# Optimization experiments

Hardware: AMD Instinct MI355X
Metric: run time of the kernel (lower is better)

The kernel has to match this reference:

```python
import jax, jax.numpy as jnp
import numpy as np

GH, GW = 7, 7            # hierarchical grid size
LN_EPS = 1e-5            # torch nn.LayerNorm default eps
NEG = -1e9


def _adaptive_avg_pool2d(x, oh, ow):
    # Replicates torch F.adaptive_avg_pool2d bin boundaries:
    # start=floor(i*H/out), end=ceil((i+1)*H/out). x: (..., H, W)
    H, W = x.shape[-2], x.shape[-1]
    def b(i, n, o):
        return int(np.floor(i * n / o)), int(np.ceil((i + 1) * n / o))
    rows = jnp.stack([x[..., b(i, H, oh)[0]:b(i, H, oh)[1], :].mean(axis=-2)
                      for i in range(oh)], axis=-2)
    out = jnp.stack([rows[..., b(j, W, ow)[0]:b(j, W, ow)[1]].mean(axis=-1)
                     for j in range(ow)], axis=-1)
    return out


def _layernorm(y, gamma, beta):
    mu = y.mean(axis=-1, keepdims=True)
    var = jnp.mean(jnp.square(y - mu), axis=-1, keepdims=True)
    return (y - mu) * jax.lax.rsqrt(var + LN_EPS) * gamma + beta


def setup_inputs() -> dict:
    key = jax.random.key(0)
    ks = jax.random.split(key, 16)
    B, C, H, W = 8, 512, 32, 32
    heads = 8
    s = 0.02
    f32 = jnp.float32
    return {
        "x":    jax.random.normal(ks[0], (B, C, H, W), f32),
        "Wq":   jax.random.normal(ks[1], (C, C), f32) * s,
        "bq":   jnp.zeros((C,), f32),
        "Wk":   jax.random.normal(ks[2], (C, C), f32) * s,
        "bk":   jnp.zeros((C,), f32),
        "Wv":   jax.random.normal(ks[3], (C, C), f32) * s,
        "bv":   jnp.zeros((C,), f32),
        "Wo":   jax.random.normal(ks[4], (C, C), f32) * s,
        "bo":   jnp.zeros((C,), f32),
        "Wsp":  jax.random.normal(ks[5], (heads, C), f32) * s,   # 1x1 conv C->heads
        "bsp":  jnp.zeros((heads,), f32),
        "Wse1": jax.random.normal(ks[6], (C // 16, C), f32) * s, # SE squeeze
        "bse1": jnp.zeros((C // 16,), f32),
        "Wse2": jax.random.normal(ks[7], (C, C // 16), f32) * s, # SE excite
        "bse2": jnp.zeros((C,), f32),
        "gamma": jnp.ones((C,), f32),
        "beta":  jnp.zeros((C,), f32),
    }


def reference(x, Wq, bq, Wk, bk, Wv, bv, Wo, bo, Wsp, bsp,
              Wse1, bse1, Wse2, bse2, gamma, beta):
    B, C, H, W = x.shape
    heads = Wsp.shape[0]
    d = C // heads
    N = H * W

    # --- hierarchical grid mask ---
    sp = jnp.einsum('bchw,nc->bnhw', x, Wsp) + bsp[None, :, None, None]
    m = jax.nn.sigmoid(sp)                               # (B, heads, H, W)
    mg = _adaptive_avg_pool2d(m, GH, GW)
    mg = (mg > 0.5).astype(x.dtype)                      # binarize
    ih = np.floor(np.arange(H) * GH / H).astype(np.int32)  # torch 'nearest'
    iw = np.floor(np.arange(W) * GW / W).astype(np.int32)
    mask = mg[..., ih[:, None], iw[None, :]]             # (B, heads, H, W)

    # --- SE channel gating ---
    pooled = x.mean(axis=(2, 3))                         # (B, C)
    h1 = jax.nn.relu(pooled @ Wse1.T + bse1)
    cw = jax.nn.sigmoid(h1 @ Wse2.T + bse2)              # (B, C)
    xf = (x * cw[:, :, None, None]).reshape(B, C, N).transpose(0, 2, 1)  # (B,N,C)

    # --- multi-head attention with outer-product additive mask ---
    def heads_split(t):
        return t.reshape(B, N, heads, d).transpose(0, 2, 1, 3)  # (B,h,N,d)
    Q = heads_split(xf @ Wq.T + bq)
    K = heads_split(xf @ Wk.T + bk)
    V = heads_split(xf @ Wv.T + bv)

    scores = jnp.einsum('bhnd,bhmd->bhnm', Q, K) / (d ** 0.5)
    mf = mask.reshape(B, heads, N)
    bias = (1.0 - mf[:, :, :, None] * mf[:, :, None, :]) * NEG
    w = jax.nn.softmax(scores + bias, axis=-1)
    attn = jnp.einsum('bhnm,bhmd->bhnd', w, V)
    attn = attn.transpose(0, 2, 1, 3).reshape(B, N, C)
    attn = attn @ Wo.T + bo

    y = _layernorm(xf + attn, gamma, beta)               # (B, N, C)
    return y.transpose(0, 2, 1).reshape(B, C, H, W)
```

## Files before the change

kernel.cpp:

```cpp
#include <hip/hip_runtime.h>
#include <hip/hip_bf16.h>
#include <math.h>

typedef unsigned short u16;
typedef unsigned int u32;
typedef __attribute__((ext_vector_type(4))) float f32x4;
typedef __attribute__((ext_vector_type(8))) short bf16x8;
typedef __attribute__((ext_vector_type(4))) unsigned short us4;
typedef __attribute__((ext_vector_type(8))) unsigned short us8;

#define DI __device__ __forceinline__

#define NEGS  (-1.4426950408889634e9f)
#define QKSCL (0.18033688011112042f)
#define DEFTH (11.541560327111708f)

DI u16 f2b(float x){ __hip_bfloat16 h = __float2bfloat16(x); return *reinterpret_cast<u16*>(&h); }
DI float b2f(u16 u){ union { float f; u32 i; } v; v.i = ((u32)u) << 16; return v.f; }

DI u32 cvtpk(float lo, float hi){
  u32 r;
  asm("v_cvt_pk_bf16_f32 %0, %1, %2" : "=v"(r) : "v"(lo), "v"(hi));
  return r;
}
DI float exp2a(float x){
  float r;
  asm("v_exp_f32 %0, %1" : "=v"(r) : "v"(x));
  return r;
}

DI void gload16(const void* g, void* l){
  __builtin_amdgcn_global_load_lds((const __attribute__((address_space(1))) void*)g,
                                   (__attribute__((address_space(3))) void*)l, 16, 0, 0);
}

__global__ void k_cvt(const float* __restrict__ Wq, const float* __restrict__ Wk,
                      const float* __restrict__ Wv, const float* __restrict__ Wo,
                      u16* __restrict__ WB, u16* __restrict__ WoB){
  int i = blockIdx.x * 256 + threadIdx.x;
  WB[i]          = f2b(Wq[i]);
  WB[262144 + i] = f2b(Wk[i]);
  WB[524288 + i] = f2b(Wv[i]);
  WoB[i]         = f2b(Wo[i]);
}

__global__ __launch_bounds__(256) void k_pooled(const float* __restrict__ x, float* __restrict__ pooled){
  int row  = blockIdx.x * 4 + (threadIdx.x >> 6);
  int lane = threadIdx.x & 63;
  const float4* p = (const float4*)(x + ((size_t)row << 10));
  float4 v0 = p[lane], v1 = p[lane + 64], v2 = p[lane + 128], v3 = p[lane + 192];
  float s = (v0.x + v0.y + v0.z + v0.w) + (v1.x + v1.y + v1.z + v1.w)
          + (v2.x + v2.y + v2.z + v2.w) + (v3.x + v3.y + v3.z + v3.w);
  #pragma unroll
  for (int o = 32; o > 0; o >>= 1) s += __shfl_down(s, o, 64);
  if (lane == 0) pooled[row] = s * (1.0f / 1024.0f);
}

__global__ __launch_bounds__(256) void k_se(const float* __restrict__ pooled,
    const float* __restrict__ Wse1, const float* __restrict__ bse1,
    const float* __restrict__ Wse2, const float* __restrict__ bse2,
    float* __restrict__ cw){
  __shared__ float pl[512];
  __shared__ float h1[32];
  int b = blockIdx.x, t = threadIdx.x;
  pl[t] = pooled[b * 512 + t];
  pl[t + 256] = pooled[b * 512 + t + 256];
  __syncthreads();
  if (t < 32){
    float acc = bse1[t];
    const float* w = Wse1 + t * 512;
    for (int c = 0; c < 512; c++) acc = fmaf(pl[c], w[c], acc);
    h1[t] = fmaxf(acc, 0.0f);
  }
  __syncthreads();
  for (int c = t; c < 512; c += 256){
    float acc = bse2[c];
    const float* w = Wse2 + c * 32;
    #pragma unroll
    for (int j = 0; j < 32; j++) acc = fmaf(h1[j], w[j], acc);
    cw[b * 512 + c] = 1.0f / (1.0f + expf(-acc));
  }
}

__global__ __launch_bounds__(256) void k_spxf(const float* __restrict__ x,
    const float* __restrict__ Wsp, const float* __restrict__ bsp,
    const float* __restrict__ cw, float* __restrict__ mbuf, u16* __restrict__ xfB){
  __shared__ float wsh[4096];
  __shared__ float cwl[512];
  __shared__ float tile[64][36];
  __shared__ float part[8][256];
  int t = threadIdx.x;
  int b = blockIdx.x >> 5, n0 = (blockIdx.x & 31) << 5;
  for (int i = t; i < 4096; i += 256) wsh[i] = Wsp[i];
  cwl[t] = cw[b * 512 + t];
  cwl[t + 256] = cw[b * 512 + t + 256];

  int nl = t & 31, cg = t >> 5;
  int lr = t >> 2, lc = (t & 3) << 3;
  float acc[8] = {0,0,0,0,0,0,0,0};

  for (int cb = 0; cb < 8; cb++){
    __syncthreads();
    const float* xp = x + ((size_t)(b * 512 + cb * 64 + lr) << 10) + n0 + lc;
    float4 v0 = *(const float4*)xp;
    float4 v1 = *(const float4*)(xp + 4);
    *(float4*)&tile[lr][lc]     = v0;
    *(float4*)&tile[lr][lc + 4] = v1;
    __syncthreads();
    float sc[8];
    #pragma unroll
    for (int i = 0; i < 8; i++){
      int c = cb * 64 + cg * 8 + i;
      float v = tile[cg * 8 + i][nl];
      sc[i] = v * cwl[c];
      #pragma unroll
      for (int h = 0; h < 8; h++) acc[h] = fmaf(v, wsh[(h << 9) + c], acc[h]);
    }
    union { u32 d[4]; us8 v; } xu;
    #pragma unroll
    for (int i = 0; i < 4; i++) xu.d[i] = cvtpk(sc[2*i], sc[2*i+1]);
    *(us8*)&xfB[(((size_t)(b * 1024 + n0 + nl)) << 9) + cb * 64 + cg * 8] = xu.v;
  }
  #pragma unroll
  for (int h = 0; h < 8; h++) part[cg][h * 32 + nl] = acc[h];
  __syncthreads();
  {
    int h = t >> 5, px = t & 31;
    float s = bsp[h];
    #pragma unroll
    for (int g2 = 0; g2 < 8; g2++) s += part[g2][h * 32 + px];
    mbuf[(((size_t)(b * 8 + h)) << 10) + n0 + px] = 1.0f / (1.0f + expf(-s));
  }
}

__global__ void k_mask(const float* __restrict__ mbuf, float* __restrict__ bneg){
  __shared__ float sm[1024];
  __shared__ float mg[49];
  int bh = blockIdx.x, t = threadIdx.x;
  const float* mp = mbuf + ((size_t)bh << 10);
  for (int i = t; i < 1024; i += 64) sm[i] = mp[i];
  __syncthreads();
  if (t < 49){
    int ci = t / 7, cj = t % 7;
    int r0 = (ci * 32) / 7, r1 = ((ci + 1) * 32 + 6) / 7;
    int c0 = (cj * 32) / 7, c1 = ((cj + 1) * 32 + 6) / 7;
    float acc = 0.0f;
    for (int cc = c0; cc < c1; cc++){
      float rs = 0.0f;
      for (int rr = r0; rr < r1; rr++) rs += sm[rr * 32 + cc];
      acc += rs / (float)(r1 - r0);
    }
    float v = acc / (float)(c1 - c0);
    mg[t] = (v > 0.5f) ? 1.0f : 0.0f;
  }
  __syncthreads();
  for (int i = t; i < 1024; i += 64){
    int r = i >> 5, c = i & 31;
    float m = mg[((r * 7) >> 5) * 7 + ((c * 7) >> 5)];
    bneg[((size_t)bh << 10) + i] = (m > 0.5f) ? 0.0f : NEGS;
  }
}

template<int MODE>
DI void gemm_body(const u16* __restrict__ A, const u16* __restrict__ Bw,
    const float* __restrict__ b0, const float* __restrict__ b1, const float* __restrict__ b2,
    u16* __restrict__ outQ, u16* __restrict__ outK, u16* __restrict__ outV, float* __restrict__ outF){
  __shared__ __align__(16) u16 smem[16384];
  int m0 = blockIdx.x * 128, n0 = blockIdx.y * 128;
  bool vblk = (MODE == 0) && (n0 >= 1024);
  int t = threadIdx.x, lane = t & 63, w = t >> 6;
  int wr = w >> 1, wc = w & 1;
  int g = lane >> 4, li = lane & 15;
  f32x4 acc[4][4];
  #pragma unroll
  for (int mt = 0; mt < 4; mt++)
    #pragma unroll
    for (int nt = 0; nt < 4; nt++) acc[mt][nt] = (f32x4){0.f, 0.f, 0.f, 0.f};

  int cof = (((lane & 3) ^ ((lane >> 3) & 3)) << 3);
  int rl = lane >> 2;
  const u16* gA = A  + (size_t)(m0 + w * 32 + rl) * 512 + cof;
  const u16* gB = Bw + (size_t)(n0 + w * 32 + rl) * 512 + cof;
  u16* lA = smem + (w * 32) * 32;
  u16* lB = smem + 4096 + (w * 32) * 32;

  #define STAGE(buf, k0)                                              \
    gload16(gA + (k0),            lA + (buf) * 8192);                 \
    gload16(gA + (k0) + 16 * 512, lA + (buf) * 8192 + 512);           \
    gload16(gB + (k0),            lB + (buf) * 8192);                 \
    gload16(gB + (k0) + 16 * 512, lB + (buf) * 8192 + 512);

  STAGE(0, 0);
  __syncthreads();

  int rsw = ((li >> 1) & 3);
  int cA = (g ^ rsw) << 3;
  int cur = 0;
  for (int ks = 0; ks < 16; ks++){
    if (ks < 15){ STAGE(cur ^ 1, (ks + 1) * 32); }
    const u16* Ac = smem + cur * 8192;
    const u16* Bc = smem + cur * 8192 + 4096;
    bf16x8 afr[4], bfr[4];
    #pragma unroll
    for (int mt = 0; mt < 4; mt++)
      afr[mt] = *(const bf16x8*)&Ac[(wr * 64 + mt * 16 + li) * 32 + cA];
    #pragma unroll
    for (int nt = 0; nt < 4; nt++)
      bfr[nt] = *(const bf16x8*)&Bc[(wc * 64 + nt * 16 + li) * 32 + cA];
    if (vblk){
      #pragma unroll
      for (int mt = 0; mt < 4; mt++)
        #pragma unroll
        for (int nt = 0; nt < 4; nt++)
          acc[mt][nt] = __builtin_amdgcn_mfma_f32_16x16x32_bf16(afr[mt], bfr[nt], acc[mt][nt], 0, 0, 0);
    } else {
      #pragma unroll
      for (int mt = 0; mt < 4; mt++)
        #pragma unroll
        for (int nt = 0; nt < 4; nt++)
          acc[mt][nt] = __builtin_amdgcn_mfma_f32_16x16x32_bf16(bfr[nt], afr[mt], acc[mt][nt], 0, 0, 0);
    }
    __syncthreads();
    cur ^= 1;
  }
  #undef STAGE

  if (MODE == 1){
    #pragma unroll
    for (int mt = 0; mt < 4; mt++){
      #pragma unroll
      for (int nt = 0; nt < 4; nt++){
        int m = m0 + wr * 64 + mt * 16 + li;
        int obase = n0 + wc * 64 + nt * 16 + (g << 2);
        float4 bias4 = *(const float4*)&b0[obase];
        float4 vo = { acc[mt][nt][0] + bias4.x, acc[mt][nt][1] + bias4.y,
                      acc[mt][nt][2] + bias4.z, acc[mt][nt][3] + bias4.w };
        *(float4*)&outF[(size_t)m * 512 + obase] = vo;
      }
    }
    return;
  }

  u16* Cl = smem;
  const float* bb = vblk ? b2 : ((n0 >> 9) ? b1 : b0);
  #pragma unroll
  for (int p = 0; p < 2; p++){
    __syncthreads();
    if (vblk){
      if (wc == p){
        #pragma unroll
        for (int mt = 0; mt < 4; mt++){
          #pragma unroll
          for (int nt = 0; nt < 4; nt++){
            int row = nt * 16 + li;
            float bias = bb[(n0 & 511) + p * 64 + row];
            int col = wr * 64 + ((mt >> 1) << 5) + (g << 3) + ((mt & 1) << 2);
            union { u32 d[2]; us4 v; } pu;
            pu.d[0] = cvtpk(acc[mt][nt][0] + bias, acc[mt][nt][1] + bias);
            pu.d[1] = cvtpk(acc[mt][nt][2] + bias, acc[mt][nt][3] + bias);
            *(us4*)&Cl[row * 136 + col] = pu.v;
          }
        }
      }
    } else {
      if (wr == p){
        #pragma unroll
        for (int mt = 0; mt < 4; mt++){
          #pragma unroll
          for (int nt = 0; nt < 4; nt++){
            int row = mt * 16 + li;
            int ob = wc * 64 + nt * 16 + (g << 2);
            float4 bias4 = *(const float4*)&bb[(n0 & 511) + ob];
            union { u32 d[2]; us4 v; } pu;
            pu.d[0] = cvtpk(acc[mt][nt][0] + bias4.x, acc[mt][nt][1] + bias4.y);
            pu.d[1] = cvtpk(acc[mt][nt][2] + bias4.z, acc[mt][nt][3] + bias4.w);
            *(us4*)&Cl[row * 136 + ob] = pu.v;
          }
        }
      }
    }
    __syncthreads();
    int r = t >> 4, ol = (t & 15) << 3;
    if (vblk){
      int b = m0 >> 10, nt0 = m0 & 1023;
      #pragma unroll
      for (int pp = 0; pp < 4; pp++){
        int rr = pp * 16 + r;
        int c = (n0 & 511) + p * 64 + rr, h = c >> 6, dv = c & 63;
        us8 v = *(us8*)&Cl[rr * 136 + ol];
        *(us8*)&outV[(((size_t)(b * 8 + h)) << 16) + ((size_t)dv << 10) + nt0 + ol] = v;
      }
    } else {
      u16* base = (n0 >> 9) ? outK : outQ;
      #pragma unroll
      for (int pp = 0; pp < 4; pp++){
        int rr = pp * 16 + r;
        int m = m0 + p * 64 + rr, b = m >> 10, n = m & 1023;
        int c = (n0 & 511) + ol, h = c >> 6, dv = c & 63;
        us8 v = *(us8*)&Cl[rr * 136 + ol];
        *(us8*)&base[(((size_t)(b * 8 + h)) << 16) + ((size_t)n << 6) + dv] = v;
      }
    }
  }
}

__global__ __launch_bounds__(256) void k_gemm_qkv(const u16* __restrict__ A, const u16* __restrict__ Bw,
    const float* __restrict__ b0, const float* __restrict__ b1, const float* __restrict__ b2,
    u16* __restrict__ outQ, u16* __restrict__ outK, u16* __restrict__ outV){
  gemm_body<0>(A, Bw, b0, b1, b2, outQ, outK, outV, nullptr);
}

__global__ __launch_bounds__(256) void k_gemm_o(const u16* __restrict__ A, const u16* __restrict__ Bw,
    const float* __restrict__ b0, float* __restrict__ outF){
  gemm_body<1>(A, Bw, b0, nullptr, nullptr, nullptr, nullptr, nullptr, outF);
}

__global__ __launch_bounds__(256) void k_flash(const u16* __restrict__ Q, const u16* __restrict__ K,
    const u16* __restrict__ Vt, const float* __restrict__ bneg, u16* __restrict__ attnB){
  __shared__ __align__(16) u16 Ks[64 * 72];
  __shared__ __align__(16) u16 Vts[64 * 72];
  __shared__ float mks[64];
  int hw = blockIdx.x;
  int bid = ((hw & 7) << 7) + (hw >> 3);
  int bh = bid >> 4, q0 = (bid & 15) << 6;
  int t = threadIdx.x, lane = t & 63, w = t >> 6;
  int g = lane >> 4, li = lane & 15;

  const u16* Kp = K  + ((size_t)bh << 16);
  const u16* Vp = Vt + ((size_t)bh << 16);
  const float* bp = bneg + ((size_t)bh << 10);

  bf16x8 qfr0, qfr1;
  {
    const u16* qrow = Q + ((size_t)bh << 16) + ((size_t)(q0 + w * 16 + li) << 6);
    qfr0 = *(const bf16x8*)(qrow + g * 8);
    qfr1 = *(const bf16x8*)(qrow + 32 + g * 8);
  }
  float bnq = bp[q0 + w * 16 + li];

  f32x4 oacc[4];
  #pragma unroll
  for (int dt = 0; dt < 4; dt++) oacc[dt] = (f32x4){0.f, 0.f, 0.f, 0.f};
  float mrun = -INFINITY, lrun = 0.0f;

  int sr = t >> 2, sc = (t & 3) << 4;
  const u16* kg = Kp + ((size_t)sr << 6) + sc;
  const u16* vg = Vp + ((size_t)sr << 10) + sc;
  uint4 kr0, kr1, vr0, vr1;
  float mr = 0.0f;
  kr0 = *(const uint4*)(kg);
  kr1 = *(const uint4*)(kg + 8);
  vr0 = *(const uint4*)(vg);
  vr1 = *(const uint4*)(vg + 8);
  if (t < 64) mr = bp[t];

  for (int kt = 0; kt < 16; kt++){
    __syncthreads();
    *(uint4*)&Ks[sr * 72 + sc]      = kr0;
    *(uint4*)&Ks[sr * 72 + sc + 8]  = kr1;
    *(uint4*)&Vts[sr * 72 + sc]     = vr0;
    *(uint4*)&Vts[sr * 72 + sc + 8] = vr1;
    if (t < 64) mks[t] = mr;
    if (kt < 15){
      kr0 = *(const uint4*)(kg + (kt + 1) * 4096);
      kr1 = *(const uint4*)(kg + (kt + 1) * 4096 + 8);
      vr0 = *(const uint4*)(vg + (kt + 1) * 64);
      vr1 = *(const uint4*)(vg + (kt + 1) * 64 + 8);
      if (t < 64) mr = bp[(kt + 1) * 64 + t];
    }
    __syncthreads();

    f32x4 sacc[4];
    #pragma unroll
    for (int mt = 0; mt < 4; mt++) sacc[mt] = (f32x4){0.f, 0.f, 0.f, 0.f};
    __builtin_amdgcn_s_setprio(1);
    #pragma unroll
    for (int mt = 0; mt < 4; mt++){
      bf16x8 kfr0 = *(bf16x8*)&Ks[(mt * 16 + li) * 72 + g * 8];
      bf16x8 kfr1 = *(bf16x8*)&Ks[(mt * 16 + li) * 72 + 32 + g * 8];
      sacc[mt] = __builtin_amdgcn_mfma_f32_16x16x32_bf16(kfr0, qfr0, sacc[mt], 0, 0, 0);
      sacc[mt] = __builtin_amdgcn_mfma_f32_16x16x32_bf16(kfr1, qfr1, sacc[mt], 0, 0, 0);
    }
    __builtin_amdgcn_s_setprio(0);

    float tm[4];
    #pragma unroll
    for (int mt = 0; mt < 4; mt++){
      float4 bk = *(const float4*)&mks[mt * 16 + g * 4];
      float s0 = fmaf(sacc[mt][0], QKSCL, fminf(bk.x, bnq));
      float s1 = fmaf(sacc[mt][1], QKSCL, fminf(bk.y, bnq));
      float s2 = fmaf(sacc[mt][2], QKSCL, fminf(bk.z, bnq));
      float s3 = fmaf(sacc[mt][3], QKSCL, fminf(bk.w, bnq));
      sacc[mt][0] = s0; sacc[mt][1] = s1; sacc[mt][2] = s2; sacc[mt][3] = s3;
      tm[mt] = fmaxf(fmaxf(s0, s1), fmaxf(s2, s3));
    }
    float tmax = fmaxf(fmaxf(tm[0], tm[1]), fmaxf(tm[2], tm[3]));
    tmax = fmaxf(tmax, __shfl_xor(tmax, 16, 64));
    tmax = fmaxf(tmax, __shfl_xor(tmax, 32, 64));

    if (!__all(tmax <= mrun + DEFTH)){
      float mnew = fmaxf(mrun, tmax);
      float scl = exp2a(mrun - mnew);
      mrun = mnew;
      lrun *= scl;
      #pragma unroll
      for (int dt = 0; dt < 4; dt++)
        #pragma unroll
        for (int j = 0; j < 4; j++) oacc[dt][j] *= scl;
    }

    float rs[4];
    #pragma unroll
    for (int mt = 0; mt < 4; mt++){
      float p0 = exp2a(sacc[mt][0] - mrun);
      float p1 = exp2a(sacc[mt][1] - mrun);
      float p2 = exp2a(sacc[mt][2] - mrun);
      float p3 = exp2a(sacc[mt][3] - mrun);
      sacc[mt][0] = p0; sacc[mt][1] = p1; sacc[mt][2] = p2; sacc[mt][3] = p3;
      rs[mt] = (p0 + p1) + (p2 + p3);
    }
    float rsum = (rs[0] + rs[1]) + (rs[2] + rs[3]);
    rsum += __shfl_xor(rsum, 16, 64);
    rsum += __shfl_xor(rsum, 32, 64);
    lrun += rsum;

    union { u32 d[4]; bf16x8 v; } u0, u1;
    u0.d[0] = cvtpk(sacc[0][0], sacc[0][1]);
    u0.d[1] = cvtpk(sacc[0][2], sacc[0][3]);
    u0.d[2] = cvtpk(sacc[1][0], sacc[1][1]);
    u0.d[3] = cvtpk(sacc[1][2], sacc[1][3]);
    u1.d[0] = cvtpk(sacc[2][0], sacc[2][1]);
    u1.d[1] = cvtpk(sacc[2][2], sacc[2][3]);
    u1.d[2] = cvtpk(sacc[3][0], sacc[3][1]);
    u1.d[3] = cvtpk(sacc[3][2], sacc[3][3]);

    __builtin_amdgcn_s_setprio(1);
    #pragma unroll
    for (int dt = 0; dt < 4; dt++){
      bf16x8 vfr0 = *(bf16x8*)&Vts[(dt * 16 + li) * 72 + g * 8];
      bf16x8 vfr1 = *(bf16x8*)&Vts[(dt * 16 + li) * 72 + 32 + g * 8];
      oacc[dt] = __builtin_amdgcn_mfma_f32_16x16x32_bf16(vfr0, u0.v, oacc[dt], 0, 0, 0);
      oacc[dt] = __builtin_amdgcn_mfma_f32_16x16x32_bf16(vfr1, u1.v, oacc[dt], 0, 0, 0);
    }
    __builtin_amdgcn_s_setprio(0);
  }

  float inv = 1.0f / lrun;
  int b = bh >> 3, h = bh & 7;
  u16* op = attnB + (((size_t)(b * 1024 + q0 + w * 16 + li)) << 9) + h * 64 + g * 4;
  #pragma unroll
  for (int dt = 0; dt < 4; dt++){
    union { u32 d[2]; us4 v; } ou;
    ou.d[0] = cvtpk(oacc[dt][0] * inv, oacc[dt][1] * inv);
    ou.d[1] = cvtpk(oacc[dt][2] * inv, oacc[dt][3] * inv);
    *(us4*)(op + dt * 16) = ou.v;
  }
}

__global__ __launch_bounds__(256) void k_ln(const u16* __restrict__ xfB, const float* __restrict__ attnO,
    const float* __restrict__ gamma, const float* __restrict__ beta, float* __restrict__ out){
  __shared__ float mu_s[64], rs_s[64];
  __shared__ float tile[64][65];
  int b = blockIdx.x >> 4, n0 = (blockIdx.x & 15) << 6;
  int t = threadIdx.x, w = t >> 6, lane = t & 63;

  for (int r = w * 16; r < w * 16 + 16; r++){
    size_t rb = ((size_t)(b * 1024 + n0 + r)) << 9;
    const float* ap = attnO + rb + lane * 8;
    const u16*  xp = xfB + rb + lane * 8;
    float4 a0 = *(const float4*)ap;
    float4 a1 = *(const float4*)(ap + 4);
    union { uint4 v; u16 u[8]; } xv; xv.v = *(const uint4*)xp;
    float v0 = a0.x + b2f(xv.u[0]), v1 = a0.y + b2f(xv.u[1]);
    float v2 = a0.z + b2f(xv.u[2]), v3 = a0.w + b2f(xv.u[3]);
    float v4 = a1.x + b2f(xv.u[4]), v5 = a1.y + b2f(xv.u[5]);
    float v6 = a1.z + b2f(xv.u[6]), v7 = a1.w + b2f(xv.u[7]);
    float s  = v0 + v1 + v2 + v3 + v4 + v5 + v6 + v7;
    float s2 = v0*v0 + v1*v1 + v2*v2 + v3*v3 + v4*v4 + v5*v5 + v6*v6 + v7*v7;
    #pragma unroll
    for (int o = 32; o > 0; o >>= 1){ s += __shfl_xor(s, o, 64); s2 += __shfl_xor(s2, o, 64); }
    if (lane == 0){
      float mu = s * (1.0f / 512.0f);
      float var = s2 * (1.0f / 512.0f) - mu * mu;
      mu_s[r] = mu;
      rs_s[r] = 1.0f / sqrtf(var + 1e-5f);
    }
  }
  __syncthreads();

  for (int ch = 0; ch < 8; ch++){
    int c0 = ch * 64;
    {
      int r = t >> 2, cp = (t & 3) << 4;
      size_t rb = (((size_t)(b * 1024 + n0 + r)) << 9) + c0 + cp;
      float mu = mu_s[r], rstd = rs_s[r];
      #pragma unroll
      for (int i2 = 0; i2 < 2; i2++){
        float4 a0 = *(const float4*)(attnO + rb + i2 * 8);
        float4 a1 = *(const float4*)(attnO + rb + i2 * 8 + 4);
        union { uint4 v; u16 u[8]; } xv; xv.v = *(const uint4*)(xfB + rb + i2 * 8);
        float vv[8] = { a0.x + b2f(xv.u[0]), a0.y + b2f(xv.u[1]), a0.z + b2f(xv.u[2]), a0.w + b2f(xv.u[3]),
                        a1.x + b2f(xv.u[4]), a1.y + b2f(xv.u[5]), a1.z + b2f(xv.u[6]), a1.w + b2f(xv.u[7]) };
        #pragma unroll
        for (int i = 0; i < 8; i++){
          int c = c0 + cp + i2 * 8 + i;
          tile[r][cp + i2 * 8 + i] = (vv[i] - mu) * rstd * gamma[c] + beta[c];
        }
      }
    }
    __syncthreads();
    {
      int cl = t >> 2, np_ = (t & 3) << 4;
      float* op = out + (((size_t)(b * 512 + c0 + cl)) << 10) + n0 + np_;
      #pragma unroll
      for (int i = 0; i < 16; i += 4){
        float4 vo = { tile[np_ + i][cl], tile[np_ + i + 1][cl], tile[np_ + i + 2][cl], tile[np_ + i + 3][cl] };
        *(float4*)(op + i) = vo;
      }
    }
    __syncthreads();
  }
}

extern "C" void kernel_launch(void* const* d_in, const int* in_sizes, int n_in,
                              void* d_out, int out_size, void* d_ws, size_t ws_size,
                              hipStream_t stream){
  (void)in_sizes; (void)n_in; (void)out_size; (void)ws_size;
  const float* x    = (const float*)d_in[0];
  const float* Wq   = (const float*)d_in[1];
  const float* bq   = (const float*)d_in[2];
  const float* Wk   = (const float*)d_in[3];
  const float* bk   = (const float*)d_in[4];
  const float* Wv   = (const float*)d_in[5];
  const float* bv   = (const float*)d_in[6];
  const float* Wo   = (const float*)d_in[7];
  const float* bo   = (const float*)d_in[8];
  const float* Wsp  = (const float*)d_in[9];
  const float* bsp  = (const float*)d_in[10];
  const float* Wse1 = (const float*)d_in[11];
  const float* bse1 = (const float*)d_in[12];
  const float* Wse2 = (const float*)d_in[13];
  const float* bse2 = (const float*)d_in[14];
  const float* gamma= (const float*)d_in[15];
  const float* beta = (const float*)d_in[16];
  float* out = (float*)d_out;

  char* ws = (char*)d_ws;
  size_t off = 0;
  auto alloc = [&](size_t bytes) -> void* {
    void* p = ws + off;
    off += (bytes + 255) & ~(size_t)255;
    return p;
  };
  u16*   WB     = (u16*)  alloc(1536 * 512 * 2);
  u16*   WoB    = (u16*)  alloc(512 * 512 * 2);
  float* pooled = (float*)alloc(4096 * 4);
  float* cw     = (float*)alloc(4096 * 4);
  float* mbuf   = (float*)alloc(65536 * 4);
  float* bneg   = (float*)alloc(65536 * 4);
  u16*   xfB    = (u16*)  alloc((size_t)8192 * 512 * 2);
  u16*   Qb     = (u16*)  alloc(8388608);
  u16*   Kb     = (u16*)  alloc(8388608);
  u16*   VtG    = (u16*)  alloc(8388608);
  u16*   attnB  = (u16*)  alloc(8388608);
  float* attnO  = (float*)Qb;

  k_cvt   <<<dim3(1024), dim3(256), 0, stream>>>(Wq, Wk, Wv, Wo, WB, WoB);
  k_pooled<<<dim3(1024), dim3(256), 0, stream>>>(x, pooled);
  k_se    <<<dim3(8),    dim3(256), 0, stream>>>(pooled, Wse1, bse1, Wse2, bse2, cw);
  k_spxf  <<<dim3(256),  dim3(256), 0, stream>>>(x, Wsp, bsp, cw, mbuf, xfB);
  k_mask  <<<dim3(64),   dim3(64),  0, stream>>>(mbuf, bneg);
  k_gemm_qkv<<<dim3(64, 12), dim3(256), 0, stream>>>(xfB, WB, bq, bk, bv, Qb, Kb, VtG);
  k_flash <<<dim3(1024), dim3(256), 0, stream>>>(Qb, Kb, VtG, bneg, attnB);
  k_gemm_o<<<dim3(64, 4), dim3(256), 0, stream>>>(attnB, WoB, bo, attnO);
  k_ln    <<<dim3(128),  dim3(256), 0, stream>>>(xfB, attnO, gamma, beta, out);
}
```

Baseline: 147.3 us.

## Double query tile per flash block, double-buffer K/V LDS, emit bf16 out-projection

```diff
diff --git a/kernel.cpp b/kernel.cpp
--- a/kernel.cpp
+++ b/kernel.cpp
@@ -164,7 +164,7 @@
 template<int MODE>
 DI void gemm_body(const u16* __restrict__ A, const u16* __restrict__ Bw,
     const float* __restrict__ b0, const float* __restrict__ b1, const float* __restrict__ b2,
-    u16* __restrict__ outQ, u16* __restrict__ outK, u16* __restrict__ outV, float* __restrict__ outF){
+    u16* __restrict__ outQ, u16* __restrict__ outK, u16* __restrict__ outV, u16* __restrict__ outO){
   __shared__ __align__(16) u16 smem[16384];
   int m0 = blockIdx.x * 128, n0 = blockIdx.y * 128;
   bool vblk = (MODE == 0) && (n0 >= 1024);
@@ -225,24 +225,8 @@
   }
   #undef STAGE
 
-  if (MODE == 1){
-    #pragma unroll
-    for (int mt = 0; mt < 4; mt++){
-      #pragma unroll
-      for (int nt = 0; nt < 4; nt++){
-        int m = m0 + wr * 64 + mt * 16 + li;
-        int obase = n0 + wc * 64 + nt * 16 + (g << 2);
-        float4 bias4 = *(const float4*)&b0[obase];
-        float4 vo = { acc[mt][nt][0] + bias4.x, acc[mt][nt][1] + bias4.y,
-                      acc[mt][nt][2] + bias4.z, acc[mt][nt][3] + bias4.w };
-        *(float4*)&outF[(size_t)m * 512 + obase] = vo;
-      }
-    }
-    return;
-  }
-
   u16* Cl = smem;
-  const float* bb = vblk ? b2 : ((n0 >> 9) ? b1 : b0);
+  const float* bb = vblk ? b2 : ((MODE == 0 && (n0 >> 9)) ? b1 : b0);
   #pragma unroll
   for (int p = 0; p < 2; p++){
     __syncthreads();
@@ -290,7 +274,7 @@
         us8 v = *(us8*)&Cl[rr * 136 + ol];
         *(us8*)&outV[(((size_t)(b * 8 + h)) << 16) + ((size_t)dv << 10) + nt0 + ol] = v;
       }
-    } else {
+    } else if (MODE == 0){
       u16* base = (n0 >> 9) ? outK : outQ;
       #pragma unroll
       for (int pp = 0; pp < 4; pp++){
@@ -300,6 +284,14 @@
         us8 v = *(us8*)&Cl[rr * 136 + ol];
         *(us8*)&base[(((size_t)(b * 8 + h)) << 16) + ((size_t)n << 6) + dv] = v;
       }
+    } else {
+      #pragma unroll
+      for (int pp = 0; pp < 4; pp++){
+        int rr = pp * 16 + r;
+        int m = m0 + p * 64 + rr;
+        us8 v = *(us8*)&Cl[rr * 136 + ol];
+        *(us8*)&outO[((size_t)m << 9) + n0 + ol] = v;
+      }
     }
   }
 }
@@ -311,18 +303,18 @@
 }
 
 __global__ __launch_bounds__(256) void k_gemm_o(const u16* __restrict__ A, const u16* __restrict__ Bw,
-    const float* __restrict__ b0, float* __restrict__ outF){
-  gemm_body<1>(A, Bw, b0, nullptr, nullptr, nullptr, nullptr, nullptr, outF);
+    const float* __restrict__ b0, u16* __restrict__ outO){
+  gemm_body<1>(A, Bw, b0, nullptr, nullptr, nullptr, nullptr, nullptr, outO);
 }
 
 __global__ __launch_bounds__(256) void k_flash(const u16* __restrict__ Q, const u16* __restrict__ K,
     const u16* __restrict__ Vt, const float* __restrict__ bneg, u16* __restrict__ attnB){
-  __shared__ __align__(16) u16 Ks[64 * 72];
-  __shared__ __align__(16) u16 Vts[64 * 72];
-  __shared__ float mks[64];
+  __shared__ __align__(16) u16 Ks[2][64 * 88];
+  __shared__ __align__(16) u16 Vts[2][64 * 88];
+  __shared__ float mks[2][64];
   int hw = blockIdx.x;
-  int bid = ((hw & 7) << 7) + (hw >> 3);
-  int bh = bid >> 4, q0 = (bid & 15) << 6;
+  int bid = ((hw & 7) << 6) + (hw >> 3);
+  int bh = bid >> 3, q0 = (bid & 7) << 7;
   int t = threadIdx.x, lane = t & 63, w = t >> 6;
   int g = lane >> 4, li = lane & 15;
 
@@ -330,37 +322,42 @@
   const u16* Vp = Vt + ((size_t)bh << 16);
   const float* bp = bneg + ((size_t)bh << 10);
 
-  bf16x8 qfr0, qfr1;
+  bf16x8 qf0a, qf1a, qf0b, qf1b;
   {
-    const u16* qrow = Q + ((size_t)bh << 16) + ((size_t)(q0 + w * 16 + li) << 6);
-    qfr0 = *(const bf16x8*)(qrow + g * 8);
-    qfr1 = *(const bf16x8*)(qrow + 32 + g * 8);
-  }
-  float bnq = bp[q0 + w * 16 + li];
-
-  f32x4 oacc[4];
+    const u16* qra = Q + ((size_t)bh << 16) + ((size_t)(q0 + w * 32 + li) << 6);
+    qf0a = *(const bf16x8*)(qra + g * 8);
+    qf1a = *(const bf16x8*)(qra + 32 + g * 8);
+    const u16* qrb = qra + (16 << 6);
+    qf0b = *(const bf16x8*)(qrb + g * 8);
+    qf1b = *(const bf16x8*)(qrb + 32 + g * 8);
+  }
+  float bnqa = bp[q0 + w * 32 + li];
+  float bnqb = bp[q0 + w * 32 + 16 + li];
+
+  f32x4 oaccA[4], oaccB[4];
   #pragma unroll
-  for (int dt = 0; dt < 4; dt++) oacc[dt] = (f32x4){0.f, 0.f, 0.f, 0.f};
-  float mrun = -INFINITY, lrun = 0.0f;
+  for (int dt = 0; dt < 4; dt++){
+    oaccA[dt] = (f32x4){0.f, 0.f, 0.f, 0.f};
+    oaccB[dt] = (f32x4){0.f, 0.f, 0.f, 0.f};
+  }
+  float mrunA = -INFINITY, lrunA = 0.0f, mrunB = -INFINITY, lrunB = 0.0f;
 
   int sr = t >> 2, sc = (t & 3) << 4;
   const u16* kg = Kp + ((size_t)sr << 6) + sc;
   const u16* vg = Vp + ((size_t)sr << 10) + sc;
-  uint4 kr0, kr1, vr0, vr1;
-  float mr = 0.0f;
-  kr0 = *(const uint4*)(kg);
-  kr1 = *(const uint4*)(kg + 8);
-  vr0 = *(const uint4*)(vg);
-  vr1 = *(const uint4*)(vg + 8);
-  if (t < 64) mr = bp[t];
+  uint4 kr0 = *(const uint4*)(kg), kr1 = *(const uint4*)(kg + 8);
+  uint4 vr0 = *(const uint4*)(vg), vr1 = *(const uint4*)(vg + 8);
+  float mr = (t < 64) ? bp[t] : 0.0f;
+
+  *(uint4*)&Ks[0][sr * 88 + sc]      = kr0;
+  *(uint4*)&Ks[0][sr * 88 + sc + 8]  = kr1;
+  *(uint4*)&Vts[0][sr * 88 + sc]     = vr0;
+  *(uint4*)&Vts[0][sr * 88 + sc + 8] = vr1;
+  if (t < 64) mks[0][t] = mr;
+  __syncthreads();
 
   for (int kt = 0; kt < 16; kt++){
-    __syncthreads();
-    *(uint4*)&Ks[sr * 72 + sc]      = kr0;
-    *(uint4*)&Ks[sr * 72 + sc + 8]  = kr1;
-    *(uint4*)&Vts[sr * 72 + sc]     = vr0;
-    *(uint4*)&Vts[sr * 72 + sc + 8] = vr1;
-    if (t < 64) mks[t] = mr;
+    int buf = kt & 1;
     if (kt < 15){
       kr0 = *(const uint4*)(kg + (kt + 1) * 4096);
       kr1 = *(const uint4*)(kg + (kt + 1) * 4096 + 8);
@@ -368,96 +365,150 @@
       vr1 = *(const uint4*)(vg + (kt + 1) * 64 + 8);
       if (t < 64) mr = bp[(kt + 1) * 64 + t];
     }
-    __syncthreads();
-
-    f32x4 sacc[4];
-    #pragma unroll
-    for (int mt = 0; mt < 4; mt++) sacc[mt] = (f32x4){0.f, 0.f, 0.f, 0.f};
+
+    f32x4 sa[4], sb[4];
+    #pragma unroll
+    for (int mt = 0; mt < 4; mt++){ sa[mt] = (f32x4){0.f,0.f,0.f,0.f}; sb[mt] = (f32x4){0.f,0.f,0.f,0.f}; }
     __builtin_amdgcn_s_setprio(1);
     #pragma unroll
     for (int mt = 0; mt < 4; mt++){
-      bf16x8 kfr0 = *(bf16x8*)&Ks[(mt * 16 + li) * 72 + g * 8];
-      bf16x8 kfr1 = *(bf16x8*)&Ks[(mt * 16 + li) * 72 + 32 + g * 8];
-      sacc[mt] = __builtin_amdgcn_mfma_f32_16x16x32_bf16(kfr0, qfr0, sacc[mt], 0, 0, 0);
-      sacc[mt] = __builtin_amdgcn_mfma_f32_16x16x32_bf16(kfr1, qfr1, sacc[mt], 0, 0, 0);
+      bf16x8 kf0 = *(bf16x8*)&Ks[buf][(mt * 16 + li) * 88 + g * 8];
+      bf16x8 kf1 = *(bf16x8*)&Ks[buf][(mt * 16 + li) * 88 + 32 + g * 8];
+      sa[mt] = __builtin_amdgcn_mfma_f32_16x16x32_bf16(kf0, qf0a, sa[mt], 0, 0, 0);
+      sa[mt] = __builtin_amdgcn_mfma_f32_16x16x32_bf16(kf1, qf1a, sa[mt], 0, 0, 0);
+      sb[mt] = __builtin_amdgcn_mfma_f32_16x16x32_bf16(kf0, qf0b, sb[mt], 0, 0, 0);
+      sb[mt] = __builtin_amdgcn_mfma_f32_16x16x32_bf16(kf1, qf1b, sb[mt], 0, 0, 0);
     }
     __builtin_amdgcn_s_setprio(0);
 
-    float tm[4];
-    #pragma unroll
-    for (int mt = 0; mt < 4; mt++){
-      float4 bk = *(const float4*)&mks[mt * 16 + g * 4];
-      float s0 = fmaf(sacc[mt][0], QKSCL, fminf(bk.x, bnq));
-      float s1 = fmaf(sacc[mt][1], QKSCL, fminf(bk.y, bnq));
-      float s2 = fmaf(sacc[mt][2], QKSCL, fminf(bk.z, bnq));
-      float s3 = fmaf(sacc[mt][3], QKSCL, fminf(bk.w, bnq));
-      sacc[mt][0] = s0; sacc[mt][1] = s1; sacc[mt][2] = s2; sacc[mt][3] = s3;
-      tm[mt] = fmaxf(fmaxf(s0, s1), fmaxf(s2, s3));
-    }
-    float tmax = fmaxf(fmaxf(tm[0], tm[1]), fmaxf(tm[2], tm[3]));
-    tmax = fmaxf(tmax, __shfl_xor(tmax, 16, 64));
-    tmax = fmaxf(tmax, __shfl_xor(tmax, 32, 64));
-
-    if (!__all(tmax <= mrun + DEFTH)){
-      float mnew = fmaxf(mrun, tmax);
-      float scl = exp2a(mrun - mnew);
-      mrun = mnew;
-      lrun *= scl;
-      #pragma unroll
-      for (int dt = 0; dt < 4; dt++)
+    union { u32 d[4]; bf16x8 v; } u0a, u1a, u0b, u1b;
+    {
+      float tm[4];
+      #pragma unroll
+      for (int mt = 0; mt < 4; mt++){
+        float4 bk = *(const float4*)&mks[buf][mt * 16 + g * 4];
+        float s0 = fmaf(sa[mt][0], QKSCL, fminf(bk.x, bnqa));
+        float s1 = fmaf(sa[mt][1], QKSCL, fminf(bk.y, bnqa));
+        float s2 = fmaf(sa[mt][2], QKSCL, fminf(bk.z, bnqa));
+        float s3 = fmaf(sa[mt][3], QKSCL, fminf(bk.w, bnqa));
+        sa[mt][0] = s0; sa[mt][1] = s1; sa[mt][2] = s2; sa[mt][3] = s3;
+        tm[mt] = fmaxf(fmaxf(s0, s1), fmaxf(s2, s3));
+      }
+      float tmax = fmaxf(fmaxf(tm[0], tm[1]), fmaxf(tm[2], tm[3]));
+      tmax = fmaxf(tmax, __shfl_xor(tmax, 16, 64));
+      tmax = fmaxf(tmax, __shfl_xor(tmax, 32, 64));
+      if (!__all(tmax <= mrunA + DEFTH)){
+        float mnew = fmaxf(mrunA, tmax);
+        float scl = exp2a(mrunA - mnew);
+        mrunA = mnew; lrunA *= scl;
         #pragma unroll
-        for (int j = 0; j < 4; j++) oacc[dt][j] *= scl;
-    }
-
-    float rs[4];
-    #pragma unroll
-    for (int mt = 0; mt < 4; mt++){
-      float p0 = exp2a(sacc[mt][0] - mrun);
-      float p1 = exp2a(sacc[mt][1] - mrun);
-      float p2 = exp2a(sacc[mt][2] - mrun);
-      float p3 = exp2a(sacc[mt][3] - mrun);
-      sacc[mt][0] = p0; sacc[mt][1] = p1; sacc[mt][2] = p2; sacc[mt][3] = p3;
-      rs[mt] = (p0 + p1) + (p2 + p3);
-    }
-    float rsum = (rs[0] + rs[1]) + (rs[2] + rs[3]);
-    rsum += __shfl_xor(rsum, 16, 64);
-    rsum += __shfl_xor(rsum, 32, 64);
-    lrun += rsum;
-
-    union { u32 d[4]; bf16x8 v; } u0, u1;
-    u0.d[0] = cvtpk(sacc[0][0], sacc[0][1]);
-    u0.d[1] = cvtpk(sacc[0][2], sacc[0][3]);
-    u0.d[2] = cvtpk(sacc[1][0], sacc[1][1]);
-    u0.d[3] = cvtpk(sacc[1][2], sacc[1][3]);
-    u1.d[0] = cvtpk(sacc[2][0], sacc[2][1]);
-    u1.d[1] = cvtpk(sacc[2][2], sacc[2][3]);
-    u1.d[2] = cvtpk(sacc[3][0], sacc[3][1]);
-    u1.d[3] = cvtpk(sacc[3][2], sacc[3][3]);
+        for (int dt = 0; dt < 4; dt++)
+          #pragma unroll
+          for (int j = 0; j < 4; j++) oaccA[dt][j] *= scl;
+      }
+      float rs[4];
+      #pragma unroll
+      for (int mt = 0; mt < 4; mt++){
+        float p0 = exp2a(sa[mt][0] - mrunA);
+        float p1 = exp2a(sa[mt][1] - mrunA);
+        float p2 = exp2a(sa[mt][2] - mrunA);
+        float p3 = exp2a(sa[mt][3] - mrunA);
+        sa[mt][0] = p0; sa[mt][1] = p1; sa[mt][2] = p2; sa[mt][3] = p3;
+        rs[mt] = (p0 + p1) + (p2 + p3);
+      }
+      float rsum = (rs[0] + rs[1]) + (rs[2] + rs[3]);
+      rsum += __shfl_xor(rsum, 16, 64);
+      rsum += __shfl_xor(rsum, 32, 64);
+      lrunA += rsum;
+      u0a.d[0] = cvtpk(sa[0][0], sa[0][1]); u0a.d[1] = cvtpk(sa[0][2], sa[0][3]);
+      u0a.d[2] = cvtpk(sa[1][0], sa[1][1]); u0a.d[3] = cvtpk(sa[1][2], sa[1][3]);
+      u1a.d[0] = cvtpk(sa[2][0], sa[2][1]); u1a.d[1] = cvtpk(sa[2][2], sa[2][3]);
+      u1a.d[2] = cvtpk(sa[3][0], sa[3][1]); u1a.d[3] = cvtpk(sa[3][2], sa[3][3]);
+    }
+    {
+      float tm[4];
+      #pragma unroll
+      for (int mt = 0; mt < 4; mt++){
+        float4 bk = *(const float4*)&mks[buf][mt * 16 + g * 4];
+        float s0 = fmaf(sb[mt][0], QKSCL, fminf(bk.x, bnqb));
+        float s1 = fmaf(sb[mt][1], QKSCL, fminf(bk.y, bnqb));
+        float s2 = fmaf(sb[mt][2], QKSCL, fminf(bk.z, bnqb));
+        float s3 = fmaf(sb[mt][3], QKSCL, fminf(bk.w, bnqb));
+        sb[mt][0] = s0; sb[mt][1] = s1; sb[mt][2] = s2; sb[mt][3] = s3;
+        tm[mt] = fmaxf(fmaxf(s0, s1), fmaxf(s2, s3));
+      }
+      float tmax = fmaxf(fmaxf(tm[0], tm[1]), fmaxf(tm[2], tm[3]));
+      tmax = fmaxf(tmax, __shfl_xor(tmax, 16, 64));
+      tmax = fmaxf(tmax, __shfl_xor(tmax, 32, 64));
+      if (!__all(tmax <= mrunB + DEFTH)){
+        float mnew = fmaxf(mrunB, tmax);
+        float scl = exp2a(mrunB - mnew);
+        mrunB = mnew; lrunB *= scl;
+        #pragma unroll
+        for (int dt = 0; dt < 4; dt++)
+          #pragma unroll
+          for (int j = 0; j < 4; j++) oaccB[dt][j] *= scl;
+      }
+      float rs[4];
+      #pragma unroll
+      for (int mt = 0; mt < 4; mt++){
+        float p0 = exp2a(sb[mt][0] - mrunB);
+        float p1 = exp2a(sb[mt][1] - mrunB);
+        float p2 = exp2a(sb[mt][2] - mrunB);
+        float p3 = exp2a(sb[mt][3] - mrunB);
+        sb[mt][0] = p0; sb[mt][1] = p1; sb[mt][2] = p2; sb[mt][3] = p3;
+        rs[mt] = (p0 + p1) + (p2 + p3);
+      }
+      float rsum = (rs[0] + rs[1]) + (rs[2] + rs[3]);
+      rsum += __shfl_xor(rsum, 16, 64);
+      rsum += __shfl_xor(rsum, 32, 64);
+      lrunB += rsum;
+      u0b.d[0] = cvtpk(sb[0][0], sb[0][1]); u0b.d[1] = cvtpk(sb[0][2], sb[0][3]);
+      u0b.d[2] = cvtpk(sb[1][0], sb[1][1]); u0b.d[3] = cvtpk(sb[1][2], sb[1][3]);
+      u1b.d[0] = cvtpk(sb[2][0], sb[2][1]); u1b.d[1] = cvtpk(sb[2][2], sb[2][3]);
+      u1b.d[2] = cvtpk(sb[3][0], sb[3][1]); u1b.d[3] = cvtpk(sb[3][2], sb[3][3]);
+    }
 
     __builtin_amdgcn_s_setprio(1);
     #pragma unroll
     for (int dt = 0; dt < 4; dt++){
-      bf16x8 vfr0 = *(bf16x8*)&Vts[(dt * 16 + li) * 72 + g * 8];
-      bf16x8 vfr1 = *(bf16x8*)&Vts[(dt * 16 + li) * 72 + 32 + g * 8];
-      oacc[dt] = __builtin_amdgcn_mfma_f32_16x16x32_bf16(vfr0, u0.v, oacc[dt], 0, 0, 0);
-      oacc[dt] = __builtin_amdgcn_mfma_f32_16x16x32_bf16(vfr1, u1.v, oacc[dt], 0, 0, 0);
+      bf16x8 vf0 = *(bf16x8*)&Vts[buf][(dt * 16 + li) * 88 + g * 8];
+      bf16x8 vf1 = *(bf16x8*)&Vts[buf][(dt * 16 + li) * 88 + 32 + g * 8];
+      oaccA[dt] = __builtin_amdgcn_mfma_f32_16x16x32_bf16(vf0, u0a.v, oaccA[dt], 0, 0, 0);
+      oaccA[dt] = __builtin_amdgcn_mfma_f32_16x16x32_bf16(vf1, u1a.v, oaccA[dt], 0, 0, 0);
+      oaccB[dt] = __builtin_amdgcn_mfma_f32_16x16x32_bf16(vf0, u0b.v, oaccB[dt], 0, 0, 0);
+      oaccB[dt] = __builtin_amdgcn_mfma_f32_16x16x32_bf16(vf1, u1b.v, oaccB[dt], 0, 0, 0);
     }
     __builtin_amdgcn_s_setprio(0);
-  }
-
-  float inv = 1.0f / lrun;
+
+    if (kt < 15){
+      int nb = buf ^ 1;
+      *(uint4*)&Ks[nb][sr * 88 + sc]      = kr0;
+      *(uint4*)&Ks[nb][sr * 88 + sc + 8]  = kr1;
+      *(uint4*)&Vts[nb][sr * 88 + sc]     = vr0;
+      *(uint4*)&Vts[nb][sr * 88 + sc + 8] = vr1;
+      if (t < 64) mks[nb][t] = mr;
+      __syncthreads();
+    }
+  }
+
   int b = bh >> 3, h = bh & 7;
-  u16* op = attnB + (((size_t)(b * 1024 + q0 + w * 16 + li)) << 9) + h * 64 + g * 4;
+  float invA = 1.0f / lrunA, invB = 1.0f / lrunB;
+  u16* opA = attnB + (((size_t)(b * 1024 + q0 + w * 32 + li)) << 9) + h * 64 + g * 4;
+  u16* opB = opA + (16 << 9);
   #pragma unroll
   for (int dt = 0; dt < 4; dt++){
-    union { u32 d[2]; us4 v; } ou;
-    ou.d[0] = cvtpk(oacc[dt][0] * inv, oacc[dt][1] * inv);
-    ou.d[1] = cvtpk(oacc[dt][2] * inv, oacc[dt][3] * inv);
-    *(us4*)(op + dt * 16) = ou.v;
-  }
-}
-
-__global__ __launch_bounds__(256) void k_ln(const u16* __restrict__ xfB, const float* __restrict__ attnO,
+    union { u32 d[2]; us4 v; } oa, ob;
+    oa.d[0] = cvtpk(oaccA[dt][0] * invA, oaccA[dt][1] * invA);
+    oa.d[1] = cvtpk(oaccA[dt][2] * invA, oaccA[dt][3] * invA);
+    ob.d[0] = cvtpk(oaccB[dt][0] * invB, oaccB[dt][1] * invB);
+    ob.d[1] = cvtpk(oaccB[dt][2] * invB, oaccB[dt][3] * invB);
+    *(us4*)(opA + dt * 16) = oa.v;
+    *(us4*)(opB + dt * 16) = ob.v;
+  }
+}
+
+__global__ __launch_bounds__(256) void k_ln(const u16* __restrict__ xfB, const u16* __restrict__ attnO,
     const float* __restrict__ gamma, const float* __restrict__ beta, float* __restrict__ out){
   __shared__ float mu_s[64], rs_s[64];
   __shared__ float tile[64][65];
@@ -466,17 +517,14 @@
 
   for (int r = w * 16; r < w * 16 + 16; r++){
     size_t rb = ((size_t)(b * 1024 + n0 + r)) << 9;
-    const float* ap = attnO + rb + lane * 8;
-    const u16*  xp = xfB + rb + lane * 8;
-    float4 a0 = *(const float4*)ap;
-    float4 a1 = *(const float4*)(ap + 4);
-    union { uint4 v; u16 u[8]; } xv; xv.v = *(const uint4*)xp;
-    float v0 = a0.x + b2f(xv.u[0]), v1 = a0.y + b2f(xv.u[1]);
-    float v2 = a0.z + b2f(xv.u[2]), v3 = a0.w + b2f(xv.u[3]);
-    float v4 = a1.x + b2f(xv.u[4]), v5 = a1.y + b2f(xv.u[5]);
-    float v6 = a1.z + b2f(xv.u[6]), v7 = a1.w + b2f(xv.u[7]);
-    float s  = v0 + v1 + v2 + v3 + v4 + v5 + v6 + v7;
-    float s2 = v0*v0 + v1*v1 + v2*v2 + v3*v3 + v4*v4 + v5*v5 + v6*v6 + v7*v7;
+    union { uint4 v; u16 u[8]; } av; av.v = *(const uint4*)(attnO + rb + lane * 8);
+    union { uint4 v; u16 u[8]; } xv; xv.v = *(const uint4*)(xfB + rb + lane * 8);
+    float s = 0.0f, s2 = 0.0f;
+    #pragma unroll
+    for (int i = 0; i < 8; i++){
+      float v = b2f(av.u[i]) + b2f(xv.u[i]);
+      s += v; s2 += v * v;
+    }
     #pragma unroll
     for (int o = 32; o > 0; o >>= 1){ s += __shfl_xor(s, o, 64); s2 += __shfl_xor(s2, o, 64); }
     if (lane == 0){
@@ -496,15 +544,13 @@
       float mu = mu_s[r], rstd = rs_s[r];
       #pragma unroll
       for (int i2 = 0; i2 < 2; i2++){
-        float4 a0 = *(const float4*)(attnO + rb + i2 * 8);
-        float4 a1 = *(const float4*)(attnO + rb + i2 * 8 + 4);
+        union { uint4 v; u16 u[8]; } av; av.v = *(const uint4*)(attnO + rb + i2 * 8);
         union { uint4 v; u16 u[8]; } xv; xv.v = *(const uint4*)(xfB + rb + i2 * 8);
-        float vv[8] = { a0.x + b2f(xv.u[0]), a0.y + b2f(xv.u[1]), a0.z + b2f(xv.u[2]), a0.w + b2f(xv.u[3]),
-                        a1.x + b2f(xv.u[4]), a1.y + b2f(xv.u[5]), a1.z + b2f(xv.u[6]), a1.w + b2f(xv.u[7]) };
         #pragma unroll
         for (int i = 0; i < 8; i++){
           int c = c0 + cp + i2 * 8 + i;
-          tile[r][cp + i2 * 8 + i] = (vv[i] - mu) * rstd * gamma[c] + beta[c];
+          float v = b2f(av.u[i]) + b2f(xv.u[i]);
+          tile[r][cp + i2 * 8 + i] = (v - mu) * rstd * gamma[c] + beta[c];
         }
       }
     }
@@ -563,7 +609,7 @@
   u16*   Kb     = (u16*)  alloc(8388608);
   u16*   VtG    = (u16*)  alloc(8388608);
   u16*   attnB  = (u16*)  alloc(8388608);
-  float* attnO  = (float*)Qb;
+  u16*   attnOb = Qb;
 
   k_cvt   <<<dim3(1024), dim3(256), 0, stream>>>(Wq, Wk, Wv, Wo, WB, WoB);
   k_pooled<<<dim3(1024), dim3(256), 0, stream>>>(x, pooled);
@@ -571,7 +617,7 @@
   k_spxf  <<<dim3(256),  dim3(256), 0, stream>>>(x, Wsp, bsp, cw, mbuf, xfB);
   k_mask  <<<dim3(64),   dim3(64),  0, stream>>>(mbuf, bneg);
   k_gemm_qkv<<<dim3(64, 12), dim3(256), 0, stream>>>(xfB, WB, bq, bk, bv, Qb, Kb, VtG);
-  k_flash <<<dim3(1024), dim3(256), 0, stream>>>(Qb, Kb, VtG, bneg, attnB);
-  k_gemm_o<<<dim3(64, 4), dim3(256), 0, stream>>>(attnB, WoB, bo, attnO);
-  k_ln    <<<dim3(128),  dim3(256), 0, stream>>>(xfB, attnO, gamma, beta, out);
-}
+  k_flash <<<dim3(512),  dim3(256), 0, stream>>>(Qb, Kb, VtG, bneg, attnB);
+  k_gemm_o<<<dim3(64, 4), dim3(256), 0, stream>>>(attnB, WoB, bo, attnOb);
+  k_ln    <<<dim3(128),  dim3(256), 0, stream>>>(xfB, attnOb, gamma, beta, out);
+}
```

New measurement: 141.7 us. 1.04x faster.
